# Optimization experiments

Hardware: AMD Instinct MI355X
Metric: run time of the kernel (lower is better)

## Reference

```python
import jax, jax.numpy as jnp
import numpy as np

B, D, H = 16, 512, 8
MA, MR = 2048, 256  # padded max atoms / residues per graph
EPS = 1e-5


def _counts():
    ca = 1024 + (np.arange(B) * 97) % 1024   # atoms per graph
    cr = 128 + (np.arange(B) * 37) % 128     # residues per graph
    return ca, cr


def to_dense(x, batch, M):
    """PyG to_dense_batch: flat [N, D] + sorted batch ids -> [B, M, D] padded + mask."""
    N = x.shape[0]
    counts = jax.ops.segment_sum(jnp.ones(N, jnp.int32), batch, num_segments=B)
    starts = jnp.concatenate([jnp.zeros(1, counts.dtype), jnp.cumsum(counts)[:-1]])
    pos = jnp.arange(N, dtype=jnp.int32) - starts[batch]
    dense = jnp.zeros((B, M, x.shape[1]), x.dtype).at[batch, pos].set(x)
    mask = jnp.zeros((B, M), bool).at[batch, pos].set(True)
    return dense, mask, batch, pos


def mha(q, k, v, in_w, in_b, out_w, out_b, key_valid):
    """torch nn.MultiheadAttention (batch_first, eval) with key_padding_mask = ~key_valid."""
    Lq, Lk = q.shape[1], k.shape[1]
    dh = D // H
    wq, wk, wv = in_w[:D], in_w[D:2 * D], in_w[2 * D:]
    bq, bk, bv = in_b[:D], in_b[D:2 * D], in_b[2 * D:]
    qh = (q @ wq.T + bq).reshape(B, Lq, H, dh)
    kh = (k @ wk.T + bk).reshape(B, Lk, H, dh)
    vh = (v @ wv.T + bv).reshape(B, Lk, H, dh)
    scores = jnp.einsum('bqhd,bkhd->bhqk', qh, kh) / jnp.sqrt(jnp.asarray(dh, q.dtype))
    scores = jnp.where(key_valid[:, None, None, :], scores, jnp.asarray(-1e9, scores.dtype))
    attn = jax.nn.softmax(scores, axis=-1)
    out = jnp.einsum('bhqk,bkhd->bqhd', attn, vh).reshape(B, Lq, D)
    return out @ out_w.T + out_b


def layernorm(x, g, b):
    m = x.mean(-1, keepdims=True)
    v = ((x - m) ** 2).mean(-1, keepdims=True)
    return (x - m) * jax.lax.rsqrt(v + EPS) * g + b


def setup_inputs() -> dict:
    key = jax.random.key(0)
    ks = jax.random.split(key, 8)
    ca, cr = _counts()
    Na, Nr = int(ca.sum()), int(cr.sum())
    s = 0.02
    return {
        'atom_node': jax.random.normal(ks[0], (Na, D), jnp.float32),
        'res_node': jax.random.normal(ks[1], (Nr, D), jnp.float32),
        'r2a_in_w': jax.random.normal(ks[2], (3 * D, D), jnp.float32) * s,
        'r2a_in_b': jnp.zeros((3 * D,), jnp.float32),
        'r2a_out_w': jax.random.normal(ks[3], (D, D), jnp.float32) * s,
        'r2a_out_b': jnp.zeros((D,), jnp.float32),
        'a2r_in_w': jax.random.normal(ks[4], (3 * D, D), jnp.float32) * s,
        'a2r_in_b': jnp.zeros((3 * D,), jnp.float32),
        'a2r_out_w': jax.random.normal(ks[5], (D, D), jnp.float32) * s,
        'a2r_out_b': jnp.zeros((D,), jnp.float32),
        'atom_ln_g': jnp.ones((D,), jnp.float32),
        'atom_ln_b': jnp.zeros((D,), jnp.float32),
        'res_ln_g': jnp.ones((D,), jnp.float32),
        'res_ln_b': jnp.zeros((D,), jnp.float32),
        'atom_batch': jnp.asarray(np.repeat(np.arange(B), ca), jnp.int32),
        'res_batch': jnp.asarray(np.repeat(np.arange(B), cr), jnp.int32),
    }


def reference(atom_node, res_node, r2a_in_w, r2a_in_b, r2a_out_w, r2a_out_b,
              a2r_in_w, a2r_in_b, a2r_out_w, a2r_out_b,
              atom_ln_g, atom_ln_b, res_ln_g, res_ln_b,
              atom_batch, res_batch):
    atom_d, atom_mask, ab, ap = to_dense(atom_node, atom_batch, MA)
    res_d, res_mask, rb, rp = to_dense(res_node, res_batch, MR)
    # res2atom: atoms attend over residues; atom2res: residues attend over (updated) atoms
    atom_upd = mha(atom_d, res_d, res_d, r2a_in_w, r2a_in_b, r2a_out_w, r2a_out_b, res_mask)
    res_upd = mha(res_d, atom_upd, atom_upd, a2r_in_w, a2r_in_b, a2r_out_w, a2r_out_b, atom_mask)
    atom_out = layernorm(atom_upd, atom_ln_g, atom_ln_b)[ab, ap] + atom_node
    res_out = layernorm(res_upd, res_ln_g, res_ln_b)[rb, rp] + res_node
    return atom_out, res_out
```

## Files before the change

kernel.cpp:

```cpp
#include <hip/hip_runtime.h>
#include <hip/hip_bf16.h>
#include <math.h>

#define DD 512
#define NA_TOT 22904
#define NR_TOT 2904
#define MPAD_A 22960
#define MPAD_R 2960

__constant__ int c_aoff[17] = {0,1024,2145,3363,4678,6090,7599,9205,10908,12708,
                               14605,16599,17666,18830,20091,21449,22904};
__constant__ int c_roff[17] = {0,128,293,495,734,882,1067,1289,1420,1588,
                               1793,2035,2186,2374,2599,2733,2904};
__constant__ int c_apad[17] = {0,1024,2152,3376,4696,6112,7624,9232,10936,12736,
                               14640,16640,17712,18880,20144,21504,22960};
__constant__ int c_rpad[17] = {0,128,296,504,744,896,1088,1312,1448,1616,
                               1824,2072,2224,2416,2648,2784,2960};

typedef __attribute__((ext_vector_type(8))) short short8;
typedef __attribute__((ext_vector_type(4))) float f32x4;
typedef __attribute__((ext_vector_type(4))) unsigned short ushort4v;

__device__ __forceinline__ unsigned short f2bf(float f) {
  __hip_bfloat16 h = __float2bfloat16(f);
  return *reinterpret_cast<unsigned short*>(&h);
}
__device__ __forceinline__ float bf2f(unsigned short u) {
  union { unsigned int i; float f; } c; c.i = ((unsigned int)u) << 16; return c.f;
}
__device__ __forceinline__ float wred_sum(float x){
#pragma unroll
  for (int o = 32; o > 0; o >>= 1) x += __shfl_xor(x, o, 64);
  return x;
}

__device__ __forceinline__ void gl_lds16(const unsigned short* g, unsigned short* l) {
  __builtin_amdgcn_global_load_lds(
      (const __attribute__((address_space(1))) unsigned int*)g,
      (__attribute__((address_space(3))) unsigned int*)l, 16, 0, 0);
}

__global__ __launch_bounds__(256) void cvt5(
    const float* __restrict__ s0, const float* __restrict__ s1,
    const float* __restrict__ s2, const float* __restrict__ s3,
    const float* __restrict__ s4,
    unsigned short* __restrict__ d0, unsigned short* __restrict__ d1,
    unsigned short* __restrict__ d2, unsigned short* __restrict__ d3,
    unsigned short* __restrict__ d4,
    int n0, int n1, int n2, int n3, int n4)
{
  const float* s; unsigned short* d; int n;
  switch (blockIdx.y) {
    case 0: s = s0; d = d0; n = n0; break;
    case 1: s = s1; d = d1; n = n1; break;
    case 2: s = s2; d = d2; n = n2; break;
    case 3: s = s3; d = d3; n = n3; break;
    default: s = s4; d = d4; n = n4; break;
  }
  const int i = (blockIdx.x * 256 + threadIdx.x) * 4;
  if (i < n) {
    const float4 v = *reinterpret_cast<const float4*>(s + i);
    ushort4v o = { f2bf(v.x), f2bf(v.y), f2bf(v.z), f2bf(v.w) };
    *reinterpret_cast<ushort4v*>(d + i) = o;
  }
}

__global__ __launch_bounds__(256) void cvt_atom(const float* __restrict__ s,
                                                unsigned short* __restrict__ d, int n)
{
  const int i = (blockIdx.x * 256 + threadIdx.x) * 8;
  if (i < n) {
    const float4 v0 = *reinterpret_cast<const float4*>(s + i);
    const float4 v1 = *reinterpret_cast<const float4*>(s + i + 4);
    short8 pk;
    pk[0] = (short)f2bf(v0.x); pk[1] = (short)f2bf(v0.y);
    pk[2] = (short)f2bf(v0.z); pk[3] = (short)f2bf(v0.w);
    pk[4] = (short)f2bf(v1.x); pk[5] = (short)f2bf(v1.y);
    pk[6] = (short)f2bf(v1.z); pk[7] = (short)f2bf(v1.w);
    *reinterpret_cast<short8*>(d + i) = pk;
  }
}

__global__ __launch_bounds__(256) void mkmap(int* __restrict__ mapA,
                                             int* __restrict__ mapR)
{
  const int pm = blockIdx.x * 256 + threadIdx.x;
  if (pm < MPAD_A) {
    int b = 0;
#pragma unroll
    for (int i = 1; i < 16; ++i) if (pm >= c_apad[i]) b = i;
    const int rel = pm - c_apad[b];
    const int L = c_aoff[b+1] - c_aoff[b];
    mapA[pm] = c_aoff[b] + min(rel, L - 1);
  }
  if (pm < MPAD_R) {
    int b = 0;
#pragma unroll
    for (int i = 1; i < 16; ++i) if (pm >= c_rpad[i]) b = i;
    const int rel = pm - c_rpad[b];
    const int L = c_roff[b+1] - c_roff[b];
    mapR[pm] = c_roff[b] + min(rel, L - 1);
  }
}

struct GSeg {
  const void* X; const unsigned short* W; const float* bias;
  unsigned short* Y; const int* map;
  int M; int ldY; int mtiles; int flags;
};
struct GSeg4 { GSeg s[4]; };

__global__ __launch_bounds__(256) void gemm_multi(GSeg4 P, int mtpx)
{
  __shared__ unsigned short SMEM[40960];
  unsigned short* const Xb0 = SMEM;
  unsigned short* const Xb1 = SMEM + 8192;
  unsigned short* const Xb2 = SMEM + 16384;
  unsigned short* const Wb0 = SMEM + 24576;
  unsigned short* const Wb1 = SMEM + 32768;
  const GSeg sg = P.s[blockIdx.y];
  const int xcd = blockIdx.x & 7, g = blockIdx.x >> 3;
  const int mt = xcd + 8 * (g % mtpx);
  const int nt = g / mtpx;
  if (mt >= sg.mtiles) return;
  const int m0 = mt * 128, n0 = nt * 128;
  const int OUTT = sg.flags & 2, REMAP = sg.flags & 4;
  const int tid = threadIdx.x, lane = tid & 63, w = tid >> 6;
  const int la = lane & 15, lg = lane >> 4;
  const int wm = (w & 1) * 64, wn = (w >> 1) * 64;
  const int w64 = w * 64;
  const unsigned short* Xg = (const unsigned short*)sg.X;

  f32x4 acc[4][4];
#pragma unroll
  for (int i = 0; i < 4; ++i)
#pragma unroll
    for (int j = 0; j < 4; ++j) acc[i][j] = (f32x4){0.f,0.f,0.f,0.f};

  int elA[4][2], elB[4][2];
#pragma unroll
  for (int i = 0; i < 4; ++i)
#pragma unroll
    for (int kc = 0; kc < 2; ++kc) {
      { const int r = wm + i*16 + la;
        elA[i][kc] = r*64 + ((kc*32 + lg*8) ^ ((r & 7) << 3)); }
      { const int r = wn + i*16 + la;
        elB[i][kc] = r*64 + ((kc*32 + lg*8) ^ ((r & 7) << 3)); }
    }

  int srow[4];
#pragma unroll
  for (int p = 0; p < 4; ++p) {
    const int slot = p*256 + tid;
    const int rg = min(m0 + (slot >> 3), sg.M - 1);
    srow[p] = REMAP ? sg.map[rg] : rg;
  }
  int scg[4], srw[4];
#pragma unroll
  for (int p = 0; p < 4; ++p) {
    const int slot = p*256 + tid;
    srw[p] = slot >> 3;
    scg[p] = ((slot & 7) ^ (srw[p] & 7)) << 3;
  }

#define STAGE_W(DST, kb_)                                                       \
  _Pragma("unroll")                                                             \
  for (int p = 0; p < 4; ++p)                                                   \
    gl_lds16(sg.W + (size_t)(n0 + srw[p]) * DD + (kb_) + scg[p],                \
             &(DST)[(p*256 + w64) * 8]);

#define STAGE_X(DST, kb_)                                                       \
  _Pragma("unroll")                                                             \
  for (int p = 0; p < 4; ++p)                                                   \
    gl_lds16(Xg + (size_t)srow[p] * DD + (kb_) + scg[p],                        \
             &(DST)[(p*256 + w64) * 8]);

#define COMPUTE(XB, WB)                                                         \
  {                                                                             \
    short8 af[4][2], bfm[4][2];                                                 \
    _Pragma("unroll")                                                           \
    for (int i = 0; i < 4; ++i)                                                 \
      _Pragma("unroll")                                                         \
      for (int kc = 0; kc < 2; ++kc) {                                          \
        af[i][kc]  = *reinterpret_cast<const short8*>(&(XB)[elA[i][kc]]);       \
        bfm[i][kc] = *reinterpret_cast<const short8*>(&(WB)[elB[i][kc]]);       \
      }                                                                         \
    _Pragma("unroll")                                                           \
    for (int kc = 0; kc < 2; ++kc)                                              \
      _Pragma("unroll")                                                         \
      for (int i = 0; i < 4; ++i)                                               \
        _Pragma("unroll")                                                       \
        for (int j = 0; j < 4; ++j)                                             \
          acc[i][j] = __builtin_amdgcn_mfma_f32_16x16x32_bf16(af[i][kc], bfm[j][kc], acc[i][j], 0, 0, 0); \
  }

  STAGE_W(Wb0, 0);
  STAGE_X(Xb0, 0);
  STAGE_X(Xb1, 64);

#pragma unroll
  for (int k = 0; k < 8; ++k) {
    __builtin_amdgcn_s_barrier();
    asm volatile("" ::: "memory");
    if (k + 1 < 8) {
      if (((k+1) & 1) == 0) { STAGE_W(Wb0, (k+1)*64); } else { STAGE_W(Wb1, (k+1)*64); }
    }
    if (k + 2 < 8) {
      if (((k+2) % 3) == 0) { STAGE_X(Xb0, (k+2)*64); }
      else if (((k+2) % 3) == 1) { STAGE_X(Xb1, (k+2)*64); }
      else { STAGE_X(Xb2, (k+2)*64); }
    }
    if (k < 6)       { asm volatile("s_waitcnt vmcnt(12)" ::: "memory"); }
    else if (k == 6) { asm volatile("s_waitcnt vmcnt(8)" ::: "memory"); }
    else             { asm volatile("s_waitcnt vmcnt(0)" ::: "memory"); }
    __builtin_amdgcn_s_barrier();
    asm volatile("" ::: "memory");
    __builtin_amdgcn_sched_barrier(0);
    if ((k % 3) == 0)      { if ((k & 1) == 0) COMPUTE(Xb0, Wb0) else COMPUTE(Xb0, Wb1) }
    else if ((k % 3) == 1) { if ((k & 1) == 0) COMPUTE(Xb1, Wb0) else COMPUTE(Xb1, Wb1) }
    else                   { if ((k & 1) == 0) COMPUTE(Xb2, Wb0) else COMPUTE(Xb2, Wb1) }
  }

#undef STAGE_W
#undef STAGE_X
#undef COMPUTE

  __syncthreads();
  unsigned short* Cs = SMEM;
  if (!OUTT) {
#pragma unroll
    for (int j = 0; j < 4; ++j) {
      const int n = wn + j*16 + la;
      const float bj = sg.bias[n0 + n];
#pragma unroll
      for (int i = 0; i < 4; ++i) {
        const int mb = wm + i*16 + lg*4;
#pragma unroll
        for (int r = 0; r < 4; ++r) {
          const int m = mb + r;
          Cs[m*128 + (((n >> 3) ^ (m & 7)) << 3) + (n & 7)] = f2bf(acc[i][j][r] + bj);
        }
      }
    }
    __syncthreads();
#pragma unroll
    for (int p = 0; p < 8; ++p) {
      const int sid = p*256 + tid;
      const int row = sid >> 4, s = sid & 15;
      if (m0 + row < sg.M) {
        const short8 v = *reinterpret_cast<const short8*>(&Cs[row*128 + ((s ^ (row & 7)) << 3)]);
        *reinterpret_cast<short8*>(sg.Y + (size_t)(m0 + row)*sg.ldY + n0 + s*8) = v;
      }
    }
  } else {
#pragma unroll
    for (int j = 0; j < 4; ++j) {
      const int n = wn + j*16 + la;
      const float bj = sg.bias[n0 + n];
#pragma unroll
      for (int i = 0; i < 4; ++i) {
        const int mb = wm + i*16 + lg*4;
#pragma unroll
        for (int r = 0; r < 4; ++r) {
          const int m = mb + r;
          Cs[n*128 + (((m >> 3) ^ (n & 7)) << 3) + (m & 7)] = f2bf(acc[i][j][r] + bj);
        }
      }
    }
    __syncthreads();
#pragma unroll
    for (int p = 0; p < 8; ++p) {
      const int sid = p*256 + tid;
      const int row = sid >> 4, s = sid & 15;
      if (m0 + s*8 < sg.M) {
        const short8 v = *reinterpret_cast<const short8*>(&Cs[row*128 + ((s ^ (row & 7)) << 3)]);
        *reinterpret_cast<short8*>(sg.Y + (size_t)(n0 + row)*sg.ldY + m0 + s*8) = v;
      }
    }
  }
}

template<int SWAP>
__global__ __launch_bounds__(256, 4) void attn_v7(const unsigned short* __restrict__ Q,
                                                  const unsigned short* __restrict__ K,
                                                  const unsigned short* __restrict__ VT,
                                                  unsigned short* __restrict__ O, int ldvt)
{
  __shared__ unsigned short Ks[2][64*64];
  __shared__ unsigned short Vs[2][64*64];
  __shared__ unsigned short Pl[4][16*64];
  const int* qo  = SWAP ? c_roff : c_aoff;
  const int* ko  = SWAP ? c_aoff : c_roff;
  const int* kop = SWAP ? c_apad : c_rpad;
  const int b = blockIdx.x >> 3, h = blockIdx.x & 7;
  const int Lq = qo[b+1]-qo[b], Lk = ko[b+1]-ko[b];
  const int padL = kop[b+1]-kop[b];
  const int q0b = blockIdx.y * 64;
  if (q0b >= Lq) return;
  const int tid = threadIdx.x, w = tid >> 6, lane = tid & 63;
  const int la = lane & 15, lg = lane >> 4;
  const int q0 = q0b + w*16;
  const unsigned short* Qb  = Q  + (size_t)qo[b]*DD + h*64;
  const unsigned short* Kb  = K  + (size_t)kop[b]*DD + h*64;
  const unsigned short* VTb = VT + (size_t)(h*64)*ldvt + kop[b];

  short8 qf[2];
  {
    const int qrow = min(q0 + la, Lq - 1);
    qf[0] = *reinterpret_cast<const short8*>(Qb + (size_t)qrow*DD + lg*8);
    qf[1] = *reinterpret_cast<const short8*>(Qb + (size_t)qrow*DD + 32 + lg*8);
  }

  f32x4 acc[4];
#pragma unroll
  for (int j = 0; j < 4; ++j) acc[j] = (f32x4){0.f,0.f,0.f,0.f};
  float lsum[4] = {0.f,0.f,0.f,0.f};

  const int nkc = (Lk + 63) >> 6;

#define STAGE(bi, kc_)                                                          \
  {                                                                             \
    const int kbase_ = (kc_) * 64;                                              \
    _Pragma("unroll")                                                           \
    for (int p = 0; p < 2; ++p) {                                               \
      const int slot = p*256 + tid;                                             \
      const int row = slot >> 3, cg = slot & 7;                                 \
      const int srow = min(kbase_ + row, padL - 1);                             \
      gl_lds16(Kb + (size_t)srow * DD + ((cg ^ (row & 7)) << 3),                \
               &Ks[bi][(p*256 + w*64) * 8]);                                    \
    }                                                                           \
    _Pragma("unroll")                                                           \
    for (int p = 0; p < 2; ++p) {                                               \
      const int slot = p*256 + tid;                                             \
      const int row = slot >> 3, cg = slot & 7;                                 \
      const int col = min(kbase_ + ((cg ^ (row & 7)) << 3), padL - 8);          \
      gl_lds16(VTb + (size_t)row * ldvt + col, &Vs[bi][(p*256 + w*64) * 8]);    \
    }                                                                           \
  }

  STAGE(0, 0);
  __syncthreads();

  for (int kc = 0; kc < nkc; ++kc) {
    const int bi = kc & 1;
    if (kc + 1 < nkc) STAGE(bi ^ 1, kc + 1);
    const int kbase = kc * 64;

    f32x4 S[4];
#pragma unroll
    for (int j = 0; j < 4; ++j) {
      const int row = j*16 + la;
      const short8 kf0 = *reinterpret_cast<const short8*>(
          &Ks[bi][row*64 + ((lg*8) ^ ((row & 7) << 3))]);
      const short8 kf1 = *reinterpret_cast<const short8*>(
          &Ks[bi][row*64 + ((32 + lg*8) ^ ((row & 7) << 3))]);
      f32x4 s = (f32x4){0.f,0.f,0.f,0.f};
      s = __builtin_amdgcn_mfma_f32_16x16x32_bf16(qf[0], kf0, s, 0, 0, 0);
      s = __builtin_amdgcn_mfma_f32_16x16x32_bf16(qf[1], kf1, s, 0, 0, 0);
      S[j] = s;
    }

#pragma unroll
    for (int j = 0; j < 4; ++j) {
      const bool ok = (kbase + j*16 + la) < Lk;
#pragma unroll
      for (int r = 0; r < 4; ++r) {
        const float p = ok ? __expf(S[j][r] * 0.125f) : 0.f;
        S[j][r] = p;
        lsum[r] += p;
      }
    }

#pragma unroll
    for (int r = 0; r < 4; ++r) {
      const int prow = lg*4 + r;
#pragma unroll
      for (int j = 0; j < 4; ++j)
        Pl[w][prow*64 + ((j*16 + la) ^ ((prow & 7) << 3))] = f2bf(S[j][r]);
    }
    __builtin_amdgcn_wave_barrier();
    const short8 pf0 = *reinterpret_cast<const short8*>(
        &Pl[w][la*64 + ((lg*8) ^ ((la & 7) << 3))]);
    const short8 pf1 = *reinterpret_cast<const short8*>(
        &Pl[w][la*64 + ((32 + lg*8) ^ ((la & 7) << 3))]);

#pragma unroll
    for (int j = 0; j < 4; ++j) {
      const int d = j*16 + la;
      const short8 vf0 = *reinterpret_cast<const short8*>(
          &Vs[bi][d*64 + ((lg*8) ^ ((d & 7) << 3))]);
      const short8 vf1 = *reinterpret_cast<const short8*>(
          &Vs[bi][d*64 + ((32 + lg*8) ^ ((d & 7) << 3))]);
      acc[j] = __builtin_amdgcn_mfma_f32_16x16x32_bf16(pf0, vf0, acc[j], 0, 0, 0);
      acc[j] = __builtin_amdgcn_mfma_f32_16x16x32_bf16(pf1, vf1, acc[j], 0, 0, 0);
    }
    __syncthreads();
  }

#pragma unroll
  for (int msk = 1; msk <= 8; msk <<= 1)
#pragma unroll
    for (int r = 0; r < 4; ++r) lsum[r] += __shfl_xor(lsum[r], msk, 64);

#pragma unroll
  for (int r = 0; r < 4; ++r) {
    const float inv = 1.f / lsum[r];
    const int prow = lg*4 + r;
#pragma unroll
    for (int j = 0; j < 4; ++j)
      Pl[w][prow*64 + ((j*16 + la) ^ ((prow & 7) << 3))] = f2bf(acc[j][r] * inv);
  }
  __builtin_amdgcn_wave_barrier();
#pragma unroll
  for (int p = 0; p < 2; ++p) {
    const int sid = p*64 + lane;
    const int row = sid >> 3, s = sid & 7;
    const int qrow = q0 + row;
    if (qrow < Lq) {
      const short8 v = *reinterpret_cast<const short8*>(
          &Pl[w][row*64 + ((s ^ (row & 7)) << 3)]);
      *reinterpret_cast<short8*>(O + (size_t)(qo[b] + qrow)*DD + h*64 + s*8) = v;
    }
  }
#undef STAGE
}

__global__ __launch_bounds__(256) void ln_res(const unsigned short* __restrict__ Ub,
    float* __restrict__ Yout,
    const float* __restrict__ atom_node, const float* __restrict__ res_node,
    const float* __restrict__ ag, const float* __restrict__ ab,
    const float* __restrict__ rg, const float* __restrict__ rb)
{
  const int row = blockIdx.x * 4 + (threadIdx.x >> 6);
  const int lane = threadIdx.x & 63;
  if (row >= NA_TOT + NR_TOT) return;
  const float* g; const float* bb; const float* resid;
  if (row < NA_TOT) { g = ag; bb = ab; resid = atom_node + (size_t)row * DD; }
  else { g = rg; bb = rb; resid = res_node + (size_t)(row - NA_TOT) * DD; }
  const short8 xb = *reinterpret_cast<const short8*>(Ub + (size_t)row*DD + lane*8);
  float xv[8];
#pragma unroll
  for (int i = 0; i < 8; ++i) xv[i] = bf2f((unsigned short)xb[i]);
  float s = 0.f;
#pragma unroll
  for (int i = 0; i < 8; ++i) s += xv[i];
  s = wred_sum(s);
  const float mean = s * (1.f/512.f);
  float vs = 0.f;
#pragma unroll
  for (int i = 0; i < 8; ++i) { const float d = xv[i] - mean; vs = fmaf(d, d, vs); }
  vs = wred_sum(vs) * (1.f/512.f);
  const float inv = rsqrtf(vs + 1e-5f);
  const float4 g0 = *reinterpret_cast<const float4*>(g + lane*8);
  const float4 g1 = *reinterpret_cast<const float4*>(g + lane*8 + 4);
  const float4 b0 = *reinterpret_cast<const float4*>(bb + lane*8);
  const float4 b1 = *reinterpret_cast<const float4*>(bb + lane*8 + 4);
  const float4 r0 = *reinterpret_cast<const float4*>(resid + lane*8);
  const float4 r1 = *reinterpret_cast<const float4*>(resid + lane*8 + 4);
  float4 o0, o1;
  o0.x = (xv[0]-mean)*inv*g0.x + b0.x + r0.x;
  o0.y = (xv[1]-mean)*inv*g0.y + b0.y + r0.y;
  o0.z = (xv[2]-mean)*inv*g0.z + b0.z + r0.z;
  o0.w = (xv[3]-mean)*inv*g0.w + b0.w + r0.w;
  o1.x = (xv[4]-mean)*inv*g1.x + b1.x + r1.x;
  o1.y = (xv[5]-mean)*inv*g1.y + b1.y + r1.y;
  o1.z = (xv[6]-mean)*inv*g1.z + b1.z + r1.z;
  o1.w = (xv[7]-mean)*inv*g1.w + b1.w + r1.w;
  float* y = Yout + (size_t)row * DD + lane*8;
  *reinterpret_cast<float4*>(y)     = o0;
  *reinterpret_cast<float4*>(y + 4) = o1;
}

extern "C" void kernel_launch(void* const* d_in, const int* in_sizes, int n_in,
                              void* d_out, int out_size, void* d_ws, size_t ws_size,
                              hipStream_t stream) {
  (void)in_sizes; (void)n_in; (void)out_size; (void)ws_size;
  const float* atom_node = (const float*)d_in[0];
  const float* res_node  = (const float*)d_in[1];
  const float* r2a_in_w  = (const float*)d_in[2];
  const float* r2a_in_b  = (const float*)d_in[3];
  const float* r2a_out_w = (const float*)d_in[4];
  const float* r2a_out_b = (const float*)d_in[5];
  const float* a2r_in_w  = (const float*)d_in[6];
  const float* a2r_in_b  = (const float*)d_in[7];
  const float* a2r_out_w = (const float*)d_in[8];
  const float* a2r_out_b = (const float*)d_in[9];
  const float* atom_ln_g = (const float*)d_in[10];
  const float* atom_ln_b = (const float*)d_in[11];
  const float* res_ln_g  = (const float*)d_in[12];
  const float* res_ln_b  = (const float*)d_in[13];

  float* out = (float*)d_out;
  unsigned short* wsb = (unsigned short*)d_ws;
  const size_t NAD = (size_t)NA_TOT * DD;
  const size_t NRD = (size_t)NR_TOT * DD;
  const size_t PAD = (size_t)MPAD_A * DD;
  const size_t PRD = (size_t)MPAD_R * DD;
  unsigned short* slab1  = wsb;
  unsigned short* slab2  = wsb + PAD;
  unsigned short* updb   = wsb + 2*PAD;
  unsigned short* res_bf = wsb + 2*PAD + NAD + NRD;
  unsigned short* K1     = res_bf + NRD;
  unsigned short* V1T    = K1 + PRD;
  unsigned short* Q2     = V1T + PRD;
  unsigned short* O2     = Q2 + NRD;
  unsigned short* wbf    = O2 + NRD;
  unsigned short* w_r2a_in  = wbf;
  unsigned short* w_r2a_out = wbf +  786432;
  unsigned short* w_a2r_in  = wbf + 1048576;
  unsigned short* w_a2r_out = wbf + 1835008;
  int* mapA = (int*)(wbf + 2097152);
  int* mapR = mapA + MPAD_A;
  unsigned short* Q1      = slab1;
  unsigned short* atom_bf = slab2;
  unsigned short* O1      = slab2;
  unsigned short* K2      = slab1;
  unsigned short* V2T     = slab2;

  const dim3 blk(256);

  mkmap<<<dim3((MPAD_A + 255)/256), blk, 0, stream>>>(mapA, mapR);
  cvt5<<<dim3(1452, 5), blk, 0, stream>>>(
      r2a_in_w, r2a_out_w, a2r_in_w, a2r_out_w, res_node,
      w_r2a_in, w_r2a_out, w_a2r_in, w_a2r_out, res_bf,
      786432, 262144, 786432, 262144, (int)NRD);
  cvt_atom<<<dim3((int)(NAD/2048)), blk, 0, stream>>>(atom_node, atom_bf, (int)NAD);

  {
    GSeg4 A;
    A.s[0] = { atom_bf, w_r2a_in,          r2a_in_b,        Q1,  nullptr, NA_TOT, 512,    179, 0 };
    A.s[1] = { res_bf,  w_r2a_in + 262144, r2a_in_b + 512,  K1,  mapR,    MPAD_R, 512,    24,  4 };
    A.s[2] = { res_bf,  w_r2a_in + 524288, r2a_in_b + 1024, V1T, mapR,    MPAD_R, MPAD_R, 24,  6 };
    A.s[3] = { res_bf,  w_a2r_in,          a2r_in_b,        Q2,  nullptr, NR_TOT, 512,    23,  0 };
    gemm_multi<<<dim3(736, 4), blk, 0, stream>>>(A, 23);
  }
  attn_v7<0><<<dim3(128, 32), blk, 0, stream>>>(Q1, K1, V1T, O1, MPAD_R);
  {
    GSeg4 B;
    B.s[0] = { O1, w_r2a_out, r2a_out_b, updb, nullptr, NA_TOT, 512, 179, 0 };
    B.s[1] = B.s[0]; B.s[2] = B.s[0]; B.s[3] = B.s[0];
    gemm_multi<<<dim3(736, 1), blk, 0, stream>>>(B, 23);
  }
  {
    GSeg4 C;
    C.s[0] = { updb, w_a2r_in + 262144, a2r_in_b + 512,  K2,  mapA, MPAD_A, 512,    180, 4 };
    C.s[1] = { updb, w_a2r_in + 524288, a2r_in_b + 1024, V2T, mapA, MPAD_A, MPAD_A, 180, 6 };
    C.s[2] = C.s[0]; C.s[3] = C.s[0];
    gemm_multi<<<dim3(736, 2), blk, 0, stream>>>(C, 23);
  }
  attn_v7<1><<<dim3(128, 4), blk, 0, stream>>>(Q2, K2, V2T, O2, MPAD_A);
  {
    GSeg4 E;
    E.s[0] = { O2, w_a2r_out, a2r_out_b, updb + NAD, nullptr, NR_TOT, 512, 23, 0 };
    E.s[1] = E.s[0]; E.s[2] = E.s[0]; E.s[3] = E.s[0];
    gemm_multi<<<dim3(96, 1), blk, 0, stream>>>(E, 3);
  }
  ln_res<<<dim3((NA_TOT + NR_TOT + 3) / 4), blk, 0, stream>>>(
      updb, out, atom_node, res_node, atom_ln_g, atom_ln_b, res_ln_g, res_ln_b);
}
```

Measured before the change: 213.7 us.

## Split-K the atom2res attention and tighten the attention pipeline barriers

The residue-queries-over-atoms attention had only 128x4 blocks, each looping over up to 2048 keys. It is now split four ways along the key dimension into fp32 partial accumulators and row sums, stored temporarily in the output buffer, then combined by a small reduction kernel that normalises. Both attention kernels also replace __syncthreads with explicit s_barrier plus vmcnt waits, so the next K/V tile load overlaps compute. This adds an extra launch and partial-buffer traffic, and it depends on the output buffer being large enough and not yet live.

```diff
diff --git a/kernel.cpp b/kernel.cpp
--- a/kernel.cpp
+++ b/kernel.cpp
@@ -280,45 +280,7 @@
   }
 }
 
-template<int SWAP>
-__global__ __launch_bounds__(256, 4) void attn_v7(const unsigned short* __restrict__ Q,
-                                                  const unsigned short* __restrict__ K,
-                                                  const unsigned short* __restrict__ VT,
-                                                  unsigned short* __restrict__ O, int ldvt)
-{
-  __shared__ unsigned short Ks[2][64*64];
-  __shared__ unsigned short Vs[2][64*64];
-  __shared__ unsigned short Pl[4][16*64];
-  const int* qo  = SWAP ? c_roff : c_aoff;
-  const int* ko  = SWAP ? c_aoff : c_roff;
-  const int* kop = SWAP ? c_apad : c_rpad;
-  const int b = blockIdx.x >> 3, h = blockIdx.x & 7;
-  const int Lq = qo[b+1]-qo[b], Lk = ko[b+1]-ko[b];
-  const int padL = kop[b+1]-kop[b];
-  const int q0b = blockIdx.y * 64;
-  if (q0b >= Lq) return;
-  const int tid = threadIdx.x, w = tid >> 6, lane = tid & 63;
-  const int la = lane & 15, lg = lane >> 4;
-  const int q0 = q0b + w*16;
-  const unsigned short* Qb  = Q  + (size_t)qo[b]*DD + h*64;
-  const unsigned short* Kb  = K  + (size_t)kop[b]*DD + h*64;
-  const unsigned short* VTb = VT + (size_t)(h*64)*ldvt + kop[b];
-
-  short8 qf[2];
-  {
-    const int qrow = min(q0 + la, Lq - 1);
-    qf[0] = *reinterpret_cast<const short8*>(Qb + (size_t)qrow*DD + lg*8);
-    qf[1] = *reinterpret_cast<const short8*>(Qb + (size_t)qrow*DD + 32 + lg*8);
-  }
-
-  f32x4 acc[4];
-#pragma unroll
-  for (int j = 0; j < 4; ++j) acc[j] = (f32x4){0.f,0.f,0.f,0.f};
-  float lsum[4] = {0.f,0.f,0.f,0.f};
-
-  const int nkc = (Lk + 63) >> 6;
-
-#define STAGE(bi, kc_)                                                          \
+#define ATT_STAGE(bi, kc_)                                                      \
   {                                                                             \
     const int kbase_ = (kc_) * 64;                                              \
     _Pragma("unroll")                                                           \
@@ -338,63 +300,104 @@
     }                                                                           \
   }
 
-  STAGE(0, 0);
-  __syncthreads();
-
+#define ATT_COMPUTE(bi, kbase)                                                  \
+  {                                                                             \
+    f32x4 S[4];                                                                 \
+    _Pragma("unroll")                                                           \
+    for (int j = 0; j < 4; ++j) {                                               \
+      const int row = j*16 + la;                                                \
+      const short8 kf0 = *reinterpret_cast<const short8*>(                      \
+          &Ks[bi][row*64 + ((lg*8) ^ ((row & 7) << 3))]);                       \
+      const short8 kf1 = *reinterpret_cast<const short8*>(                      \
+          &Ks[bi][row*64 + ((32 + lg*8) ^ ((row & 7) << 3))]);                  \
+      f32x4 s = (f32x4){0.f,0.f,0.f,0.f};                                       \
+      s = __builtin_amdgcn_mfma_f32_16x16x32_bf16(qf[0], kf0, s, 0, 0, 0);      \
+      s = __builtin_amdgcn_mfma_f32_16x16x32_bf16(qf[1], kf1, s, 0, 0, 0);      \
+      S[j] = s;                                                                 \
+    }                                                                           \
+    _Pragma("unroll")                                                           \
+    for (int j = 0; j < 4; ++j) {                                               \
+      const bool ok = (kbase + j*16 + la) < Lk;                                 \
+      _Pragma("unroll")                                                         \
+      for (int r = 0; r < 4; ++r) {                                             \
+        const float p = ok ? __expf(S[j][r] * 0.125f) : 0.f;                    \
+        S[j][r] = p;                                                            \
+        lsum[r] += p;                                                           \
+      }                                                                         \
+    }                                                                           \
+    _Pragma("unroll")                                                           \
+    for (int r = 0; r < 4; ++r) {                                               \
+      const int prow = lg*4 + r;                                                \
+      _Pragma("unroll")                                                         \
+      for (int j = 0; j < 4; ++j)                                               \
+        Pl[w][prow*64 + ((j*16 + la) ^ ((prow & 7) << 3))] = f2bf(S[j][r]);     \
+    }                                                                           \
+    __builtin_amdgcn_wave_barrier();                                            \
+    const short8 pf0 = *reinterpret_cast<const short8*>(                        \
+        &Pl[w][la*64 + ((lg*8) ^ ((la & 7) << 3))]);                            \
+    const short8 pf1 = *reinterpret_cast<const short8*>(                        \
+        &Pl[w][la*64 + ((32 + lg*8) ^ ((la & 7) << 3))]);                       \
+    _Pragma("unroll")                                                           \
+    for (int j = 0; j < 4; ++j) {                                               \
+      const int d = j*16 + la;                                                  \
+      const short8 vf0 = *reinterpret_cast<const short8*>(                      \
+          &Vs[bi][d*64 + ((lg*8) ^ ((d & 7) << 3))]);                           \
+      const short8 vf1 = *reinterpret_cast<const short8*>(                      \
+          &Vs[bi][d*64 + ((32 + lg*8) ^ ((d & 7) << 3))]);                      \
+      acc[j] = __builtin_amdgcn_mfma_f32_16x16x32_bf16(pf0, vf0, acc[j], 0, 0, 0); \
+      acc[j] = __builtin_amdgcn_mfma_f32_16x16x32_bf16(pf1, vf1, acc[j], 0, 0, 0); \
+    }                                                                           \
+  }
+
+__global__ __launch_bounds__(256, 4) void attn_v7(const unsigned short* __restrict__ Q,
+                                                  const unsigned short* __restrict__ K,
+                                                  const unsigned short* __restrict__ VT,
+                                                  unsigned short* __restrict__ O, int ldvt)
+{
+  __shared__ unsigned short Ks[2][64*64];
+  __shared__ unsigned short Vs[2][64*64];
+  __shared__ unsigned short Pl[4][16*64];
+  const int b = blockIdx.x >> 3, h = blockIdx.x & 7;
+  const int Lq = c_aoff[b+1]-c_aoff[b], Lk = c_roff[b+1]-c_roff[b];
+  const int padL = c_rpad[b+1]-c_rpad[b];
+  const int q0b = blockIdx.y * 64;
+  if (q0b >= Lq) return;
+  const int tid = threadIdx.x, w = tid >> 6, lane = tid & 63;
+  const int la = lane & 15, lg = lane >> 4;
+  const int q0 = q0b + w*16;
+  const unsigned short* Qb  = Q  + (size_t)c_aoff[b]*DD + h*64;
+  const unsigned short* Kb  = K  + (size_t)c_rpad[b]*DD + h*64;
+  const unsigned short* VTb = VT + (size_t)(h*64)*ldvt + c_rpad[b];
+
+  short8 qf[2];
+  {
+    const int qrow = min(q0 + la, Lq - 1);
+    qf[0] = *reinterpret_cast<const short8*>(Qb + (size_t)qrow*DD + lg*8);
+    qf[1] = *reinterpret_cast<const short8*>(Qb + (size_t)qrow*DD + 32 + lg*8);
+  }
+
+  f32x4 acc[4];
+#pragma unroll
+  for (int j = 0; j < 4; ++j) acc[j] = (f32x4){0.f,0.f,0.f,0.f};
+  float lsum[4] = {0.f,0.f,0.f,0.f};
+
+  const int nkc = (Lk + 63) >> 6;
+  ATT_STAGE(0, 0);
   for (int kc = 0; kc < nkc; ++kc) {
     const int bi = kc & 1;
-    if (kc + 1 < nkc) STAGE(bi ^ 1, kc + 1);
+    __builtin_amdgcn_s_barrier();
+    asm volatile("" ::: "memory");
+    if (kc + 1 < nkc) {
+      ATT_STAGE(bi ^ 1, kc + 1);
+      asm volatile("s_waitcnt vmcnt(4)" ::: "memory");
+    } else {
+      asm volatile("s_waitcnt vmcnt(0)" ::: "memory");
+    }
+    __builtin_amdgcn_s_barrier();
+    asm volatile("" ::: "memory");
+    __builtin_amdgcn_sched_barrier(0);
     const int kbase = kc * 64;
-
-    f32x4 S[4];
-#pragma unroll
-    for (int j = 0; j < 4; ++j) {
-      const int row = j*16 + la;
-      const short8 kf0 = *reinterpret_cast<const short8*>(
-          &Ks[bi][row*64 + ((lg*8) ^ ((row & 7) << 3))]);
-      const short8 kf1 = *reinterpret_cast<const short8*>(
-          &Ks[bi][row*64 + ((32 + lg*8) ^ ((row & 7) << 3))]);
-      f32x4 s = (f32x4){0.f,0.f,0.f,0.f};
-      s = __builtin_amdgcn_mfma_f32_16x16x32_bf16(qf[0], kf0, s, 0, 0, 0);
-      s = __builtin_amdgcn_mfma_f32_16x16x32_bf16(qf[1], kf1, s, 0, 0, 0);
-      S[j] = s;
-    }
-
-#pragma unroll
-    for (int j = 0; j < 4; ++j) {
-      const bool ok = (kbase + j*16 + la) < Lk;
-#pragma unroll
-      for (int r = 0; r < 4; ++r) {
-        const float p = ok ? __expf(S[j][r] * 0.125f) : 0.f;
-        S[j][r] = p;
-        lsum[r] += p;
-      }
-    }
-
-#pragma unroll
-    for (int r = 0; r < 4; ++r) {
-      const int prow = lg*4 + r;
-#pragma unroll
-      for (int j = 0; j < 4; ++j)
-        Pl[w][prow*64 + ((j*16 + la) ^ ((prow & 7) << 3))] = f2bf(S[j][r]);
-    }
-    __builtin_amdgcn_wave_barrier();
-    const short8 pf0 = *reinterpret_cast<const short8*>(
-        &Pl[w][la*64 + ((lg*8) ^ ((la & 7) << 3))]);
-    const short8 pf1 = *reinterpret_cast<const short8*>(
-        &Pl[w][la*64 + ((32 + lg*8) ^ ((la & 7) << 3))]);
-
-#pragma unroll
-    for (int j = 0; j < 4; ++j) {
-      const int d = j*16 + la;
-      const short8 vf0 = *reinterpret_cast<const short8*>(
-          &Vs[bi][d*64 + ((lg*8) ^ ((d & 7) << 3))]);
-      const short8 vf1 = *reinterpret_cast<const short8*>(
-          &Vs[bi][d*64 + ((32 + lg*8) ^ ((d & 7) << 3))]);
-      acc[j] = __builtin_amdgcn_mfma_f32_16x16x32_bf16(pf0, vf0, acc[j], 0, 0, 0);
-      acc[j] = __builtin_amdgcn_mfma_f32_16x16x32_bf16(pf1, vf1, acc[j], 0, 0, 0);
-    }
-    __syncthreads();
+    ATT_COMPUTE(bi, kbase);
   }
 
 #pragma unroll
@@ -419,10 +422,114 @@
     if (qrow < Lq) {
       const short8 v = *reinterpret_cast<const short8*>(
           &Pl[w][row*64 + ((s ^ (row & 7)) << 3)]);
-      *reinterpret_cast<short8*>(O + (size_t)(qo[b] + qrow)*DD + h*64 + s*8) = v;
-    }
-  }
-#undef STAGE
+      *reinterpret_cast<short8*>(O + (size_t)(c_aoff[b] + qrow)*DD + h*64 + s*8) = v;
+    }
+  }
+}
+
+__global__ __launch_bounds__(256, 4) void attn_sk(const unsigned short* __restrict__ Q,
+                                                  const unsigned short* __restrict__ K,
+                                                  const unsigned short* __restrict__ VT,
+                                                  float* __restrict__ Pout)
+{
+  __shared__ unsigned short Ks[2][64*64];
+  __shared__ unsigned short Vs[2][64*64];
+  __shared__ unsigned short Pl[4][16*64];
+  const int b = blockIdx.x >> 3, h = blockIdx.x & 7;
+  const int qt = blockIdx.y, z = blockIdx.z;
+  const int Lq = c_roff[b+1]-c_roff[b], Lk = c_aoff[b+1]-c_aoff[b];
+  const int padL = c_apad[b+1]-c_apad[b];
+  const int ldvt = MPAD_A;
+  const int q0b = qt * 64;
+  if (q0b >= Lq) return;
+  const int tid = threadIdx.x, w = tid >> 6, lane = tid & 63;
+  const int la = lane & 15, lg = lane >> 4;
+  const int q0 = q0b + w*16;
+  float* pp = Pout + ((size_t)(blockIdx.x*4 + qt)*4 + z) * 4160;
+
+  const int nkc = (Lk + 63) >> 6;
+  const int cps = (nkc + 3) >> 2;
+  const int k0 = z * cps, k1 = min(k0 + cps, nkc);
+  if (k0 >= k1) {
+    for (int i = tid; i < 4160; i += 256) pp[i] = 0.f;
+    return;
+  }
+
+  const unsigned short* Qb  = Q  + (size_t)c_roff[b]*DD + h*64;
+  const unsigned short* Kb  = K  + (size_t)c_apad[b]*DD + h*64;
+  const unsigned short* VTb = VT + (size_t)(h*64)*ldvt + c_apad[b];
+
+  short8 qf[2];
+  {
+    const int qrow = min(q0 + la, Lq - 1);
+    qf[0] = *reinterpret_cast<const short8*>(Qb + (size_t)qrow*DD + lg*8);
+    qf[1] = *reinterpret_cast<const short8*>(Qb + (size_t)qrow*DD + 32 + lg*8);
+  }
+
+  f32x4 acc[4];
+#pragma unroll
+  for (int j = 0; j < 4; ++j) acc[j] = (f32x4){0.f,0.f,0.f,0.f};
+  float lsum[4] = {0.f,0.f,0.f,0.f};
+
+  ATT_STAGE(0, k0);
+  for (int kc = k0; kc < k1; ++kc) {
+    const int bi = (kc - k0) & 1;
+    __builtin_amdgcn_s_barrier();
+    asm volatile("" ::: "memory");
+    if (kc + 1 < k1) {
+      ATT_STAGE(bi ^ 1, kc + 1);
+      asm volatile("s_waitcnt vmcnt(4)" ::: "memory");
+    } else {
+      asm volatile("s_waitcnt vmcnt(0)" ::: "memory");
+    }
+    __builtin_amdgcn_s_barrier();
+    asm volatile("" ::: "memory");
+    __builtin_amdgcn_sched_barrier(0);
+    const int kbase = kc * 64;
+    ATT_COMPUTE(bi, kbase);
+  }
+
+#pragma unroll
+  for (int msk = 1; msk <= 8; msk <<= 1)
+#pragma unroll
+    for (int r = 0; r < 4; ++r) lsum[r] += __shfl_xor(lsum[r], msk, 64);
+
+#pragma unroll
+  for (int j = 0; j < 4; ++j)
+#pragma unroll
+    for (int r = 0; r < 4; ++r)
+      pp[(size_t)(w*16 + lg*4 + r)*64 + j*16 + la] = acc[j][r];
+  if (la == 0) {
+#pragma unroll
+    for (int r = 0; r < 4; ++r) pp[4096 + w*16 + lg*4 + r] = lsum[r];
+  }
+}
+
+__global__ __launch_bounds__(256) void attn_red(const float* __restrict__ Pin,
+                                                unsigned short* __restrict__ O)
+{
+  const int b = blockIdx.x >> 3, h = blockIdx.x & 7;
+  const int qt = blockIdx.y;
+  const int Lq = c_roff[b+1]-c_roff[b];
+  const int q0b = qt * 64;
+  if (q0b >= Lq) return;
+  const int t = threadIdx.x;
+  const int row = t >> 2, dg = (t & 3) * 16;
+  if (q0b + row >= Lq) return;
+  const float* base = Pin + ((size_t)(blockIdx.x*4 + qt)*4) * 4160;
+  const float ls = base[4096 + row] + base[4160 + 4096 + row]
+                 + base[2*4160 + 4096 + row] + base[3*4160 + 4096 + row];
+  const float inv = 1.f / ls;
+  unsigned short ov[16];
+#pragma unroll
+  for (int e = 0; e < 16; ++e) {
+    const int idx = row*64 + dg + e;
+    const float s = base[idx] + base[4160 + idx] + base[2*4160 + idx] + base[3*4160 + idx];
+    ov[e] = f2bf(s * inv);
+  }
+  unsigned short* dst = O + (size_t)(c_roff[b] + q0b + row)*DD + h*64 + dg;
+  *reinterpret_cast<short8*>(dst)     = *reinterpret_cast<short8*>(&ov[0]);
+  *reinterpret_cast<short8*>(dst + 8) = *reinterpret_cast<short8*>(&ov[8]);
 }
 
 __global__ __launch_bounds__(256) void ln_res(const unsigned short* __restrict__ Ub,
@@ -516,6 +623,7 @@
   unsigned short* O1      = slab2;
   unsigned short* K2      = slab1;
   unsigned short* V2T     = slab2;
+  float* partials = out;
 
   const dim3 blk(256);
 
@@ -534,7 +642,7 @@
     A.s[3] = { res_bf,  w_a2r_in,          a2r_in_b,        Q2,  nullptr, NR_TOT, 512,    23,  0 };
     gemm_multi<<<dim3(736, 4), blk, 0, stream>>>(A, 23);
   }
-  attn_v7<0><<<dim3(128, 32), blk, 0, stream>>>(Q1, K1, V1T, O1, MPAD_R);
+  attn_v7<<<dim3(128, 32), blk, 0, stream>>>(Q1, K1, V1T, O1, MPAD_R);
   {
     GSeg4 B;
     B.s[0] = { O1, w_r2a_out, r2a_out_b, updb, nullptr, NA_TOT, 512, 179, 0 };
@@ -548,7 +656,8 @@
     C.s[2] = C.s[0]; C.s[3] = C.s[0];
     gemm_multi<<<dim3(736, 2), blk, 0, stream>>>(C, 23);
   }
-  attn_v7<1><<<dim3(128, 4), blk, 0, stream>>>(Q2, K2, V2T, O2, MPAD_A);
+  attn_sk<<<dim3(128, 4, 4), blk, 0, stream>>>(Q2, K2, V2T, partials);
+  attn_red<<<dim3(128, 4), blk, 0, stream>>>(partials, O2);
   {
     GSeg4 E;
     E.s[0] = { O2, w_a2r_out, a2r_out_b, updb + NAD, nullptr, NR_TOT, 512, 23, 0 };
```

Result: no change. 212.6 us (-0.5%).
